# Optimization experiments

Measured on AMD Instinct MI355X. Metric: run time of the kernel, lower is better.

Reference implementation:

```python
import jax, jax.numpy as jnp
import numpy as np

N = 50000      # nodes
E = 800000     # directed edges
GNN_DIM = 128  # node feature dim
HID = 64       # per-head hidden dim of conv1
HEADS = 2
OUT = 16       # output_dim (classes)
TEXT = 500     # tf-idf text dim
M = 10000      # masked / labeled nodes


def setup_inputs() -> dict:
    key = jax.random.key(0)
    ks = jax.random.split(key, 32)
    w = lambda k, s: jax.random.normal(k, s, jnp.float32) * 0.05
    inp = {
        'text_features': jax.random.normal(ks[0], (M, TEXT), jnp.float32),
        'x': jax.random.normal(ks[1], (N, GNN_DIM), jnp.float32),
        'edge_index': jax.random.randint(ks[2], (2, E), 0, N),
        'mask': jax.random.randint(ks[3], (M,), 0, N),
        # text MLP (Linear stored as [in, out])
        'fc1_w': w(ks[4], (TEXT, 128)), 'fc1_b': w(ks[5], (128,)),
        'fc2_w': w(ks[6], (128, 64)),  'fc2_b': w(ks[7], (64,)),
        'fc3_w': w(ks[8], (64, 16)),   'fc3_b': w(ks[9], (16,)),
        'fc4_w': w(ks[10], (16, OUT)), 'fc4_b': w(ks[11], (OUT,)),
        'sc_w': w(ks[12], (TEXT, OUT)), 'sc_b': w(ks[13], (OUT,)),
        # GATConv1: in=GNN_DIM, heads=2, out=HID, concat=True
        'W1': w(ks[14], (GNN_DIM, HEADS * HID)),
        'att_src1': w(ks[15], (HEADS, HID)), 'att_dst1': w(ks[16], (HEADS, HID)),
        'b1': w(ks[17], (HEADS * HID,)),
        # GATConv2: in=2*HID, heads=1, out=OUT, concat=False
        'W2': w(ks[18], (HEADS * HID, OUT)),
        'att_src2': w(ks[19], (1, OUT)), 'att_dst2': w(ks[20], (1, OUT)),
        'b2': w(ks[21], (OUT,)),
        # fc_final: [2*OUT, OUT]
        'fcf_w': w(ks[22], (2 * OUT, OUT)), 'fcf_b': w(ks[23], (OUT,)),
    }
    return inp


def _gat_layer(h_in, src, dst, W, a_src, a_dst, b, heads, dim, concat):
    # PyG GATConv (default negative_slope=0.2, self-loops already appended)
    n = h_in.shape[0]
    h = (h_in @ W).reshape(n, heads, dim)                      # [N,H,D]
    a_s = jnp.einsum('nhd,hd->nh', h, a_src)                   # [N,H]
    a_d = jnp.einsum('nhd,hd->nh', h, a_dst)
    e = jax.nn.leaky_relu(a_s[src] + a_d[dst], 0.2)            # [E,H]
    emax = jax.ops.segment_max(e, dst, num_segments=n)
    ex = jnp.exp(e - emax[dst])
    den = jax.ops.segment_sum(ex, dst, num_segments=n)
    alpha = ex / (den[dst] + 1e-16)                            # [E,H]
    msg = h[src] * alpha[:, :, None]                           # [E,H,D]
    out = jax.ops.segment_sum(msg, dst, num_segments=n)        # [N,H,D]
    out = out.reshape(n, heads * dim) if concat else out.mean(axis=1)
    return out + b


def reference(text_features, x, edge_index, mask,
              fc1_w, fc1_b, fc2_w, fc2_b, fc3_w, fc3_b, fc4_w, fc4_b,
              sc_w, sc_b, W1, att_src1, att_dst1, b1,
              W2, att_src2, att_dst2, b2, fcf_w, fcf_b):
    n = x.shape[0]
    loop = jnp.arange(n, dtype=edge_index.dtype)
    src = jnp.concatenate([edge_index[0], loop])
    dst = jnp.concatenate([edge_index[1], loop])

    # GNN branch
    g = jax.nn.relu(_gat_layer(x, src, dst, W1, att_src1, att_dst1, b1,
                               HEADS, HID, True))
    g = _gat_layer(g, src, dst, W2, att_src2, att_dst2, b2, 1, OUT, False)
    gnn_out = g[mask]                                          # [M,OUT]

    # text MLP branch with shortcut
    t = jax.nn.relu(text_features @ fc1_w + fc1_b)
    t = jax.nn.relu(t @ fc2_w + fc2_b)
    t = jax.nn.relu(t @ fc3_w + fc3_b)
    text_out = (t @ fc4_w + fc4_b) + (text_features @ sc_w + sc_b)  # [M,OUT]

    combined = jnp.concatenate([text_out, gnn_out], axis=1)    # [M,2*OUT]
    return jax.nn.log_softmax(combined @ fcf_w + fcf_b, axis=1)
```

## Files before the change

kernel.cpp:

```cpp
#include <hip/hip_runtime.h>
#include <hip/hip_bf16.h>
#include <cmath>

#define TEXTD 500
#define GNN_DIM 128
#define DEGP(v) ((v) << 5)

typedef __attribute__((ext_vector_type(8))) short bf16x8;
typedef __attribute__((ext_vector_type(4))) float f32x4;

__device__ __forceinline__ float bf2f(unsigned short u) {
    union { unsigned int i; float f; } cv;
    cv.i = ((unsigned int)u) << 16;
    return cv.f;
}
__device__ __forceinline__ unsigned short f2b(float x) {
    __hip_bfloat16 b = __float2bfloat16(x);
    return *reinterpret_cast<unsigned short*>(&b);
}
__device__ __forceinline__ float u2f(unsigned int u) {
    union { unsigned int i; float f; } cv; cv.i = u; return cv.f;
}
__device__ __forceinline__ bf16x8 cvt8(const float* p) {
    float4 u = *(const float4*)p;
    float4 v = *(const float4*)(p + 4);
    bf16x8 f;
    f[0] = (short)f2b(u.x); f[1] = (short)f2b(u.y);
    f[2] = (short)f2b(u.z); f[3] = (short)f2b(u.w);
    f[4] = (short)f2b(v.x); f[5] = (short)f2b(v.y);
    f[6] = (short)f2b(v.z); f[7] = (short)f2b(v.w);
    return f;
}

__global__ __launch_bounds__(256) void setup_kernel(
    int* __restrict__ deg, int N, int NB,
    const float* __restrict__ fc1_w, const float* __restrict__ sc_w,
    const float* __restrict__ W1, const float* __restrict__ W2,
    unsigned short* __restrict__ w1cat, unsigned short* __restrict__ w1g,
    unsigned short* __restrict__ w2t)
{
    if ((int)blockIdx.x < NB) {
        int v = blockIdx.x * 256 + threadIdx.x;
        if (v < N) deg[DEGP(v)] = 0;
        return;
    }
    int idx = (blockIdx.x - NB) * 256 + threadIdx.x;
    if (idx < 144 * 512) {
        int n = idx >> 9, k = idx & 511;
        float v = 0.f;
        if (k < TEXTD) v = (n < 128) ? fc1_w[k * 128 + n] : sc_w[k * 16 + (n - 128)];
        w1cat[idx] = f2b(v);
    } else if (idx < 144 * 512 + 128 * 128) {
        int j = idx - 144 * 512;
        int n = j >> 7, k = j & 127;
        w1g[j] = f2b(W1[k * 128 + n]);
    } else if (idx < 144 * 512 + 128 * 128 + 16 * 128) {
        int j = idx - (144 * 512 + 128 * 128);
        int n = j >> 7, k = j & 127;
        w2t[j] = f2b(W2[k * 16 + n]);
    }
}

__global__ __launch_bounds__(256) void text_fused_kernel(
    const float* __restrict__ text, const short* __restrict__ B,
    const float* __restrict__ fc1_b, const float* __restrict__ sc_b,
    const float* __restrict__ fc2_w, const float* __restrict__ fc2_b,
    const float* __restrict__ fc3_w, const float* __restrict__ fc3_b,
    const float* __restrict__ fc4_w, const float* __restrict__ fc4_b,
    float* __restrict__ text_out, int M)
{
    __shared__ float t1s[64][128];
    __shared__ float tscs[64][16];
    __shared__ float t2s[64][64];
    __shared__ float t3s[64][16];

    const int tid = threadIdx.x;
    const int wave = tid >> 6, lane = tid & 63;
    const int q = lane >> 4, col = lane & 15;
    const int mb = blockIdx.x * 64;
    const int rbase = wave * 16;
    const int arow = min(mb + rbase + col, M - 1);
    const float* ap = text + (size_t)arow * TEXTD + q * 8;

    bf16x8 afrag[16];
    #pragma unroll
    for (int ks = 0; ks < 15; ks++) afrag[ks] = cvt8(ap + ks * 32);
    {
        bf16x8 f;
        int k0 = 480 + q * 8;
        #pragma unroll
        for (int e = 0; e < 8; e++) {
            int k = k0 + e;
            f[e] = (short)((k < TEXTD) ? f2b(text[(size_t)arow * TEXTD + k]) : 0);
        }
        afrag[15] = f;
    }

    for (int nb = 0; nb < 9; nb++) {
        const short* bp = B + (size_t)(nb * 16 + col) * 512 + q * 8;
        f32x4 acc = {0.f, 0.f, 0.f, 0.f};
        #pragma unroll
        for (int ks = 0; ks < 16; ks++)
            acc = __builtin_amdgcn_mfma_f32_16x16x32_bf16(afrag[ks], *(const bf16x8*)(bp + ks * 32), acc, 0, 0, 0);
        #pragma unroll
        for (int i = 0; i < 4; i++) {
            int rl = rbase + q * 4 + i;
            if (nb < 8) t1s[rl][nb * 16 + col] = fmaxf(acc[i] + fc1_b[nb * 16 + col], 0.f);
            else        tscs[rl][col] = acc[i] + sc_b[col];
        }
    }
    __syncthreads();

    const int c2 = tid & 63, rg2 = tid >> 6;
    for (int rb = 0; rb < 16; rb++) {
        int row = rb * 4 + rg2;
        float a2 = fc2_b[c2];
        for (int k = 0; k < 128; k++) a2 = fmaf(t1s[row][k], fc2_w[k * 64 + c2], a2);
        t2s[row][c2] = fmaxf(a2, 0.f);
    }
    __syncthreads();

    const int cs = tid & 15, rg3 = tid >> 4;
    for (int rb = 0; rb < 4; rb++) {
        int row = rb * 16 + rg3;
        float a3 = fc3_b[cs];
        for (int k = 0; k < 64; k++) a3 = fmaf(t2s[row][k], fc3_w[k * 16 + cs], a3);
        t3s[row][cs] = fmaxf(a3, 0.f);
    }
    __syncthreads();

    for (int rb = 0; rb < 4; rb++) {
        int row = rb * 16 + rg3;
        float a4 = fc4_b[cs];
        #pragma unroll
        for (int k = 0; k < 16; k++) a4 = fmaf(t3s[row][k], fc4_w[k * 16 + cs], a4);
        int rg = mb + row;
        if (rg < M) text_out[(size_t)rg * 16 + cs] = a4 + tscs[row][cs];
    }
}

__global__ __launch_bounds__(256) void gemm_h1_kernel(
    const float* __restrict__ x, const short* __restrict__ B,
    const float* __restrict__ as1w, const float* __restrict__ ad1w,
    unsigned short* __restrict__ h1, float* __restrict__ a_s, float* __restrict__ a_d, int N)
{
    const int tid = threadIdx.x;
    const int wave = tid >> 6, lane = tid & 63;
    const int q = lane >> 4, col = lane & 15;
    const int mb = blockIdx.x * 64 + wave * 16;
    const int arow = min(mb + col, N - 1);
    const float* ap = x + (size_t)arow * 128 + q * 8;

    bf16x8 afrag[4];
    #pragma unroll
    for (int ks = 0; ks < 4; ks++) afrag[ks] = cvt8(ap + ks * 32);

    float ps0[4] = {0,0,0,0}, ps1[4] = {0,0,0,0};
    float pd0[4] = {0,0,0,0}, pd1[4] = {0,0,0,0};

    #pragma unroll
    for (int nb = 0; nb < 8; nb++) {
        const short* bp = B + (size_t)(nb * 16 + col) * 128 + q * 8;
        f32x4 acc = {0.f, 0.f, 0.f, 0.f};
        #pragma unroll
        for (int ks = 0; ks < 4; ks++)
            acc = __builtin_amdgcn_mfma_f32_16x16x32_bf16(afrag[ks], *(const bf16x8*)(bp + ks * 32), acc, 0, 0, 0);
        const int j = nb * 16 + col;
        const float asj = as1w[j], adj = ad1w[j];
        #pragma unroll
        for (int i = 0; i < 4; i++) {
            int row = mb + q * 4 + i;
            if (row < N) h1[(size_t)row * 128 + j] = f2b(acc[i]);
            if (nb < 4) { ps0[i] = fmaf(acc[i], asj, ps0[i]); pd0[i] = fmaf(acc[i], adj, pd0[i]); }
            else        { ps1[i] = fmaf(acc[i], asj, ps1[i]); pd1[i] = fmaf(acc[i], adj, pd1[i]); }
        }
    }
    #pragma unroll
    for (int i = 0; i < 4; i++) {
        float v0 = ps0[i], v1 = ps1[i], w0 = pd0[i], w1 = pd1[i];
        #pragma unroll
        for (int off = 1; off < 16; off <<= 1) {
            v0 += __shfl_xor(v0, off, 16);
            v1 += __shfl_xor(v1, off, 16);
            w0 += __shfl_xor(w0, off, 16);
            w1 += __shfl_xor(w1, off, 16);
        }
        int row = mb + q * 4 + i;
        if (col == 0 && row < N) {
            a_s[2 * row] = v0; a_s[2 * row + 1] = v1;
            a_d[2 * row] = w0; a_d[2 * row + 1] = w1;
        }
    }
}

__global__ __launch_bounds__(256) void deg_hist_kernel(
    const int* __restrict__ edst, int* __restrict__ deg, int* __restrict__ rank, int E)
{
    const int base = blockIdx.x * 1024 + threadIdx.x;
    int e0 = base;
    int e1 = base + 256;
    int e2 = base + 512;
    int e3 = base + 768;
    int d0 = (e0 < E) ? edst[e0] : -1;
    int d1 = (e1 < E) ? edst[e1] : -1;
    int d2 = (e2 < E) ? edst[e2] : -1;
    int d3 = (e3 < E) ? edst[e3] : -1;
    int r0 = (d0 >= 0) ? atomicAdd(&deg[DEGP(d0)], 1) : 0;
    int r1 = (d1 >= 0) ? atomicAdd(&deg[DEGP(d1)], 1) : 0;
    int r2 = (d2 >= 0) ? atomicAdd(&deg[DEGP(d2)], 1) : 0;
    int r3 = (d3 >= 0) ? atomicAdd(&deg[DEGP(d3)], 1) : 0;
    if (d0 >= 0) rank[e0] = r0;
    if (d1 >= 0) rank[e1] = r1;
    if (d2 >= 0) rank[e2] = r2;
    if (d3 >= 0) rank[e3] = r3;
}

__global__ __launch_bounds__(256) void part_kernel(
    const int* __restrict__ deg, int* __restrict__ bsum, int N)
{
    const int tid = threadIdx.x;
    int i = blockIdx.x * 256 + tid;
    int d = (i < N) ? deg[DEGP(i)] + 1 : 0;
    #pragma unroll
    for (int off = 32; off > 0; off >>= 1) d += __shfl_down(d, off, 64);
    __shared__ int wsum[4];
    if ((tid & 63) == 0) wsum[tid >> 6] = d;
    __syncthreads();
    if (tid == 0) bsum[blockIdx.x] = wsum[0] + wsum[1] + wsum[2] + wsum[3];
}

__global__ __launch_bounds__(256) void rowptr_kernel(
    const int* __restrict__ deg, const int* __restrict__ bsum,
    int* __restrict__ rowptr, int N, int NB)
{
    __shared__ int bsc[256];
    __shared__ int sc[256];
    const int tid = threadIdx.x;

    int bv = (tid < NB) ? bsum[tid] : 0;
    bsc[tid] = bv;
    for (int off = 1; off < 256; off <<= 1) {
        __syncthreads();
        int t = (tid >= off) ? bsc[tid - off] : 0;
        __syncthreads();
        bsc[tid] += t;
    }
    __syncthreads();
    const int base = (blockIdx.x == 0) ? 0 : bsc[blockIdx.x - 1];

    const int i = blockIdx.x * 256 + tid;
    int d = (i < N) ? deg[DEGP(i)] + 1 : 0;
    sc[tid] = d;
    for (int off = 1; off < 256; off <<= 1) {
        __syncthreads();
        int t = (tid >= off) ? sc[tid - off] : 0;
        __syncthreads();
        sc[tid] += t;
    }
    __syncthreads();
    int incl = sc[tid];
    if (i < N) rowptr[i] = base + incl - d;
    if (i == N - 1) rowptr[N] = base + incl;
}

__device__ __forceinline__ float edge_w(float e) {
    return __expf(e > 0.f ? e : 0.2f * e);
}

__global__ __launch_bounds__(256) void fillw_kernel(
    const int* __restrict__ esrc, const int* __restrict__ edst,
    const int* __restrict__ rank, const int* __restrict__ rowptr,
    uint2* __restrict__ eslot,
    const float* __restrict__ a_s, const float* __restrict__ a_d, int E, int N)
{
    int e = blockIdx.x * 256 + threadIdx.x;
    if (e < E) {
        int src = esrc[e], dst = edst[e];
        int pos = rowptr[dst] + 1 + rank[e];
        float2 as = *(const float2*)(a_s + 2 * src);
        float2 ad = *(const float2*)(a_d + 2 * dst);
        unsigned int w0 = f2b(edge_w(as.x + ad.x));
        unsigned int w1 = f2b(edge_w(as.y + ad.y));
        uint2 o; o.x = (unsigned int)src; o.y = (w1 << 16) | w0;
        eslot[pos] = o;
    } else if (e < E + N) {
        int v = e - E;
        float2 as = *(const float2*)(a_s + 2 * v);
        float2 ad = *(const float2*)(a_d + 2 * v);
        unsigned int w0 = f2b(edge_w(as.x + ad.x));
        unsigned int w1 = f2b(edge_w(as.y + ad.y));
        uint2 o; o.x = (unsigned int)v; o.y = (w1 << 16) | w0;
        eslot[rowptr[v]] = o;
    }
}

template<int B>
__device__ __forceinline__ void gat1_batch(
    int i0, int end, int endm1, int wsh,
    const uint2* __restrict__ eslot, const uint2* __restrict__ h1u, unsigned int dp,
    float& a0, float& a1, float& a2, float& a3, float& den)
{
    int ics[B];
    uint2 sl[B];
    float wv[B];
    uint2 hv[B];
    #pragma unroll
    for (int k = 0; k < B; k++) ics[k] = min(i0 + 2 * k, endm1);
    #pragma unroll
    for (int k = 0; k < B; k++) sl[k] = eslot[ics[k]];
    #pragma unroll
    for (int k = 0; k < B; k++) {
        float w = u2f((sl[k].y << wsh) & 0xffff0000u);
        wv[k] = (i0 + 2 * k < end) ? w : 0.f;
    }
    #pragma unroll
    for (int k = 0; k < B; k++) hv[k] = h1u[(sl[k].x << 5) | dp];
    #pragma unroll
    for (int k = 0; k < B; k++) {
        float w = wv[k];
        den += w;
        a0 = fmaf(w, u2f(hv[k].x << 16),          a0);
        a1 = fmaf(w, u2f(hv[k].x & 0xffff0000u),  a1);
        a2 = fmaf(w, u2f(hv[k].y << 16),          a2);
        a3 = fmaf(w, u2f(hv[k].y & 0xffff0000u),  a3);
    }
}

__global__ __launch_bounds__(256) void gat1_gather_kernel(
    const int* __restrict__ rowptr, const uint2* __restrict__ eslot,
    const uint2* __restrict__ h1u,
    const float* __restrict__ b1, uint2* __restrict__ g1b, int N)
{
    const int v = blockIdx.x * 4 + (threadIdx.x >> 6);
    if (v >= N) return;
    const int lane = threadIdx.x & 63;
    const int slot = lane >> 5;
    const unsigned int dp = lane & 31;
    const int head = dp >> 4;
    const int wsh = head ? 0 : 16;
    const int beg = rowptr[v], end = rowptr[v + 1];
    const int deg = end - beg;
    const int endm1 = end - 1;
    const int i0 = beg + slot;

    float a0 = 0.f, a1 = 0.f, a2 = 0.f, a3 = 0.f, den = 0.f;

    if (deg <= 8) {
        gat1_batch<4>(i0, end, endm1, wsh, eslot, h1u, dp, a0, a1, a2, a3, den);
    } else {
        gat1_batch<8>(i0, end, endm1, wsh, eslot, h1u, dp, a0, a1, a2, a3, den);
        for (int base = i0 + 16; base < end; base += 8)
            gat1_batch<4>(base, end, endm1, wsh, eslot, h1u, dp, a0, a1, a2, a3, den);
    }

    a0 += __shfl_xor(a0, 32, 64);
    a1 += __shfl_xor(a1, 32, 64);
    a2 += __shfl_xor(a2, 32, 64);
    a3 += __shfl_xor(a3, 32, 64);
    den += __shfl_xor(den, 32, 64);

    if (lane < 32) {
        float inv = 1.f / (den + 1e-16f);
        float4 bv = *(const float4*)(b1 + 4 * dp);
        float o0 = fmaxf(fmaf(a0, inv, bv.x), 0.f);
        float o1 = fmaxf(fmaf(a1, inv, bv.y), 0.f);
        float o2 = fmaxf(fmaf(a2, inv, bv.z), 0.f);
        float o3 = fmaxf(fmaf(a3, inv, bv.w), 0.f);
        uint2 o;
        o.x = ((unsigned int)f2b(o1) << 16) | f2b(o0);
        o.y = ((unsigned int)f2b(o3) << 16) | f2b(o2);
        g1b[((unsigned int)v << 5) | dp] = o;
    }
}

__global__ __launch_bounds__(256) void gat2_proj_kernel(
    const unsigned short* __restrict__ g1b, const short* __restrict__ w2t,
    const float* __restrict__ as2w, const float* __restrict__ ad2w,
    float* __restrict__ h2, float* __restrict__ a_s2, float* __restrict__ a_d2, int N)
{
    const int tid = threadIdx.x;
    const int wave = tid >> 6, lane = tid & 63;
    const int q = lane >> 4, col = lane & 15;
    const int mb = blockIdx.x * 64 + wave * 16;
    const int arow = min(mb + col, N - 1);
    const short* ap = (const short*)g1b + (size_t)arow * 128 + q * 8;
    const short* bp = w2t + (size_t)col * 128 + q * 8;

    f32x4 acc = {0.f, 0.f, 0.f, 0.f};
    #pragma unroll
    for (int ks = 0; ks < 4; ks++)
        acc = __builtin_amdgcn_mfma_f32_16x16x32_bf16(
            *(const bf16x8*)(ap + ks * 32), *(const bf16x8*)(bp + ks * 32), acc, 0, 0, 0);

    const float asj = as2w[col], adj = ad2w[col];
    #pragma unroll
    for (int i = 0; i < 4; i++) {
        int row = mb + q * 4 + i;
        float ps = acc[i] * asj, pd = acc[i] * adj;
        #pragma unroll
        for (int off = 1; off < 16; off <<= 1) {
            ps += __shfl_xor(ps, off, 16);
            pd += __shfl_xor(pd, off, 16);
        }
        if (row < N) {
            h2[(size_t)row * 16 + col] = acc[i];
            if (col == 0) { a_s2[row] = ps; a_d2[row] = pd; }
        }
    }
}

__global__ __launch_bounds__(256) void gat2_final_kernel(
    const int* __restrict__ rowptr, const uint2* __restrict__ eslot,
    const float* __restrict__ h2,
    const float* __restrict__ a_s2, const float* __restrict__ a_d2,
    const float* __restrict__ b2, const int* __restrict__ mask,
    const float* __restrict__ text_out,
    const float* __restrict__ fcf_w, const float* __restrict__ fcf_b,
    float* __restrict__ out, int M)
{
    const int tid = threadIdx.x;
    const int m = blockIdx.x * 4 + (tid >> 6);
    if (m >= M) return;
    const int lane = tid & 63, slot = lane >> 4, c = lane & 15;
    const int v = mask[m];
    const float adv = a_d2[v];
    const int beg = rowptr[v], end = rowptr[v + 1];
    const int i0 = beg + slot;

    float acc = 0.f, den = 0.f;
    unsigned int idxs[8];
    float msk[8], as_[8], hval[8];
    #pragma unroll
    for (int k = 0; k < 8; k++) {
        int i = i0 + 4 * k;
        int ic = min(i, end - 1);
        idxs[k] = eslot[ic].x;
        msk[k] = (i < end) ? 1.f : 0.f;
    }
    #pragma unroll
    for (int k = 0; k < 8; k++) as_[k] = a_s2[idxs[k]];
    #pragma unroll
    for (int k = 0; k < 8; k++) hval[k] = h2[(idxs[k] << 4) | (unsigned)c];
    #pragma unroll
    for (int k = 0; k < 8; k++) {
        float e = as_[k] + adv;
        float w = msk[k] * __expf(e > 0.f ? e : 0.2f * e);
        den += w;
        acc = fmaf(w, hval[k], acc);
    }
    for (int i = i0 + 32; i < end; i += 4) {
        unsigned int src = eslot[i].x;
        float e = a_s2[src] + adv;
        float w = __expf(e > 0.f ? e : 0.2f * e);
        den += w;
        acc = fmaf(w, h2[(src << 4) | (unsigned)c], acc);
    }

    acc += __shfl_xor(acc, 16, 64);
    acc += __shfl_xor(acc, 32, 64);
    den += __shfl_xor(den, 16, 64);
    den += __shfl_xor(den, 32, 64);

    if (slot == 0) {
        float gval = acc / (den + 1e-16f) + b2[c];
        float tval = text_out[(size_t)m * 16 + c];

        float logit = fcf_b[c];
        #pragma unroll
        for (int k = 0; k < 16; k++) {
            logit = fmaf(__shfl(tval, k, 16), fcf_w[k * 16 + c], logit);
            logit = fmaf(__shfl(gval, k, 16), fcf_w[(16 + k) * 16 + c], logit);
        }
        float mx = logit;
        #pragma unroll
        for (int off = 8; off > 0; off >>= 1) mx = fmaxf(mx, __shfl_xor(mx, off, 16));
        float se = expf(logit - mx);
        #pragma unroll
        for (int off = 8; off > 0; off >>= 1) se += __shfl_xor(se, off, 16);
        out[(size_t)m * 16 + c] = logit - mx - logf(se);
    }
}

extern "C" void kernel_launch(void* const* d_in, const int* in_sizes, int n_in,
                              void* d_out, int out_size, void* d_ws, size_t ws_size,
                              hipStream_t stream)
{
    const float* text  = (const float*)d_in[0];
    const float* x     = (const float*)d_in[1];
    const int*   ei    = (const int*)  d_in[2];
    const int*   mask  = (const int*)  d_in[3];
    const float* fc1_w = (const float*)d_in[4];  const float* fc1_b = (const float*)d_in[5];
    const float* fc2_w = (const float*)d_in[6];  const float* fc2_b = (const float*)d_in[7];
    const float* fc3_w = (const float*)d_in[8];  const float* fc3_b = (const float*)d_in[9];
    const float* fc4_w = (const float*)d_in[10]; const float* fc4_b = (const float*)d_in[11];
    const float* sc_w  = (const float*)d_in[12]; const float* sc_b  = (const float*)d_in[13];
    const float* W1    = (const float*)d_in[14];
    const float* as1w  = (const float*)d_in[15]; const float* ad1w  = (const float*)d_in[16];
    const float* b1    = (const float*)d_in[17];
    const float* W2    = (const float*)d_in[18];
    const float* as2w  = (const float*)d_in[19]; const float* ad2w  = (const float*)d_in[20];
    const float* b2    = (const float*)d_in[21];
    const float* fcf_w = (const float*)d_in[22]; const float* fcf_b = (const float*)d_in[23];

    const int M  = in_sizes[3];
    const int N  = in_sizes[1] / GNN_DIM;
    const int E  = in_sizes[2] / 2;
    const int EP = E + N;
    const int* esrc = ei;
    const int* edst = ei + E;

    const int Mp = ((M + 63) / 64) * 64;
    const int Np = ((N + 63) / 64) * 64;
    const int NB = (N + 255) / 256;

    float* ws = (float*)d_ws;
    size_t off = 0;
    auto alloc = [&](size_t n) { float* p = ws + off; off += (n + 63) & ~size_t(63); return p; };

    unsigned short* h1    = (unsigned short*)alloc((size_t)Np * 64);
    unsigned int*   g1b   = (unsigned int*)  alloc((size_t)N * 64);
    unsigned short* w1cat = (unsigned short*)alloc(144 * 256);
    unsigned short* w1g   = (unsigned short*)alloc(128 * 64);
    unsigned short* w2t   = (unsigned short*)alloc(16 * 64);
    float* a_s1     = alloc((size_t)2 * N);
    float* a_d1     = alloc((size_t)2 * N);
    float* h2       = alloc((size_t)N * 16);
    float* a_s2     = alloc(N);
    float* a_d2     = alloc(N);
    float* text_out = alloc((size_t)M * 16);
    uint2* eslot    = (uint2*)alloc((size_t)2 * EP);
    int* deg        = (int*)alloc((size_t)N * 32);
    int* rank       = (int*)alloc(E);
    int* rowptr     = (int*)alloc(N + 1);
    int* bsum       = (int*)alloc(256);

    const int convBlocks = (144 * 512 + 128 * 128 + 16 * 128 + 255) / 256;

    setup_kernel<<<NB + convBlocks, 256, 0, stream>>>(
        deg, N, NB, fc1_w, sc_w, W1, W2, w1cat, w1g, w2t);

    deg_hist_kernel<<<(E + 1023) / 1024, 256, 0, stream>>>(edst, deg, rank, E);
    part_kernel<<<NB, 256, 0, stream>>>(deg, bsum, N);
    rowptr_kernel<<<NB, 256, 0, stream>>>(deg, bsum, rowptr, N, NB);

    gemm_h1_kernel<<<Np / 64, 256, 0, stream>>>(
        x, (const short*)w1g, as1w, ad1w, h1, a_s1, a_d1, N);

    fillw_kernel<<<(E + N + 255) / 256, 256, 0, stream>>>(
        esrc, edst, rank, rowptr, eslot, a_s1, a_d1, E, N);

    text_fused_kernel<<<Mp / 64, 256, 0, stream>>>(
        text, (const short*)w1cat, fc1_b, sc_b,
        fc2_w, fc2_b, fc3_w, fc3_b, fc4_w, fc4_b, text_out, M);

    gat1_gather_kernel<<<(N + 3) / 4, 256, 0, stream>>>(
        rowptr, eslot, (const uint2*)h1, b1, (uint2*)g1b, N);

    gat2_proj_kernel<<<Np / 64, 256, 0, stream>>>(
        (const unsigned short*)g1b, (const short*)w2t, as2w, ad2w, h2, a_s2, a_d2, N);

    gat2_final_kernel<<<(M + 3) / 4, 256, 0, stream>>>(
        rowptr, eslot, h2, a_s2, a_d2, b2, mask, text_out, fcf_w, fcf_b,
        (float*)d_out, M);
}
```

Measured before the change: 189.3 us.

## Run text MLP layers fc2-fc4 on MFMA with one-wave blocks

Replaces the scalar FMA loops for fc2, fc3 and fc4 in the text branch with bf16 MFMA tiles. The transposed bf16 weights for these layers are prepared in the setup kernel. The text kernel is reshaped to one 64-thread wave per 16 rows, with bf16 intermediates held in small padded LDS buffers. This is meant to cut the scalar-ALU-bound tail of the text MLP and raise block count. In exchange it adds bf16 rounding to the intermediate activations and runs 625 blocks of a single wave each.

```diff
diff --git a/kernel.cpp b/kernel.cpp
--- a/kernel.cpp
+++ b/kernel.cpp
@@ -36,8 +36,11 @@
     int* __restrict__ deg, int N, int NB,
     const float* __restrict__ fc1_w, const float* __restrict__ sc_w,
     const float* __restrict__ W1, const float* __restrict__ W2,
+    const float* __restrict__ fc2_w, const float* __restrict__ fc3_w,
+    const float* __restrict__ fc4_w,
     unsigned short* __restrict__ w1cat, unsigned short* __restrict__ w1g,
-    unsigned short* __restrict__ w2t)
+    unsigned short* __restrict__ w2t, unsigned short* __restrict__ fc2t,
+    unsigned short* __restrict__ fc3t, unsigned short* __restrict__ fc4t)
 {
     if ((int)blockIdx.x < NB) {
         int v = blockIdx.x * 256 + threadIdx.x;
@@ -45,41 +48,51 @@
         return;
     }
     int idx = (blockIdx.x - NB) * 256 + threadIdx.x;
-    if (idx < 144 * 512) {
+    if (idx < 73728) {
         int n = idx >> 9, k = idx & 511;
         float v = 0.f;
         if (k < TEXTD) v = (n < 128) ? fc1_w[k * 128 + n] : sc_w[k * 16 + (n - 128)];
         w1cat[idx] = f2b(v);
-    } else if (idx < 144 * 512 + 128 * 128) {
-        int j = idx - 144 * 512;
+    } else if (idx < 90112) {
+        int j = idx - 73728;
         int n = j >> 7, k = j & 127;
         w1g[j] = f2b(W1[k * 128 + n]);
-    } else if (idx < 144 * 512 + 128 * 128 + 16 * 128) {
-        int j = idx - (144 * 512 + 128 * 128);
+    } else if (idx < 92160) {
+        int j = idx - 90112;
         int n = j >> 7, k = j & 127;
         w2t[j] = f2b(W2[k * 16 + n]);
-    }
-}
-
-__global__ __launch_bounds__(256) void text_fused_kernel(
-    const float* __restrict__ text, const short* __restrict__ B,
+    } else if (idx < 100352) {
+        int j = idx - 92160;
+        int n = j >> 7, k = j & 127;
+        fc2t[j] = f2b(fc2_w[k * 64 + n]);
+    } else if (idx < 101376) {
+        int j = idx - 100352;
+        int n = j >> 6, k = j & 63;
+        fc3t[j] = f2b(fc3_w[k * 16 + n]);
+    } else if (idx < 101888) {
+        int j = idx - 101376;
+        int n = j >> 5, k = j & 31;
+        fc4t[j] = f2b((k < 16) ? fc4_w[k * 16 + n] : 0.f);
+    }
+}
+
+__global__ __launch_bounds__(64) void text_mfma_kernel(
+    const float* __restrict__ text, const short* __restrict__ w1cat,
     const float* __restrict__ fc1_b, const float* __restrict__ sc_b,
-    const float* __restrict__ fc2_w, const float* __restrict__ fc2_b,
-    const float* __restrict__ fc3_w, const float* __restrict__ fc3_b,
-    const float* __restrict__ fc4_w, const float* __restrict__ fc4_b,
+    const short* __restrict__ fc2t, const float* __restrict__ fc2_b,
+    const short* __restrict__ fc3t, const float* __restrict__ fc3_b,
+    const short* __restrict__ fc4t, const float* __restrict__ fc4_b,
     float* __restrict__ text_out, int M)
 {
-    __shared__ float t1s[64][128];
-    __shared__ float tscs[64][16];
-    __shared__ float t2s[64][64];
-    __shared__ float t3s[64][16];
-
-    const int tid = threadIdx.x;
-    const int wave = tid >> 6, lane = tid & 63;
+    __shared__ unsigned short t1b[16 * 136];
+    __shared__ unsigned short t2b[16 * 72];
+    __shared__ unsigned short t3b[16 * 40];
+    __shared__ float tscs[16 * 16];
+
+    const int lane = threadIdx.x;
     const int q = lane >> 4, col = lane & 15;
-    const int mb = blockIdx.x * 64;
-    const int rbase = wave * 16;
-    const int arow = min(mb + rbase + col, M - 1);
+    const int mb = blockIdx.x * 16;
+    const int arow = min(mb + col, M - 1);
     const float* ap = text + (size_t)arow * TEXTD + q * 8;
 
     bf16x8 afrag[16];
@@ -97,45 +110,66 @@
     }
 
     for (int nb = 0; nb < 9; nb++) {
-        const short* bp = B + (size_t)(nb * 16 + col) * 512 + q * 8;
+        const short* bp = w1cat + (size_t)(nb * 16 + col) * 512 + q * 8;
         f32x4 acc = {0.f, 0.f, 0.f, 0.f};
         #pragma unroll
         for (int ks = 0; ks < 16; ks++)
             acc = __builtin_amdgcn_mfma_f32_16x16x32_bf16(afrag[ks], *(const bf16x8*)(bp + ks * 32), acc, 0, 0, 0);
         #pragma unroll
         for (int i = 0; i < 4; i++) {
-            int rl = rbase + q * 4 + i;
-            if (nb < 8) t1s[rl][nb * 16 + col] = fmaxf(acc[i] + fc1_b[nb * 16 + col], 0.f);
-            else        tscs[rl][col] = acc[i] + sc_b[col];
+            int row = q * 4 + i;
+            if (nb < 8) t1b[row * 136 + nb * 16 + col] = f2b(fmaxf(acc[i] + fc1_b[nb * 16 + col], 0.f));
+            else        tscs[row * 16 + col] = acc[i] + sc_b[col];
         }
     }
     __syncthreads();
 
-    const int c2 = tid & 63, rg2 = tid >> 6;
-    for (int rb = 0; rb < 16; rb++) {
-        int row = rb * 4 + rg2;
-        float a2 = fc2_b[c2];
-        for (int k = 0; k < 128; k++) a2 = fmaf(t1s[row][k], fc2_w[k * 64 + c2], a2);
-        t2s[row][c2] = fmaxf(a2, 0.f);
+    const unsigned short* a2p = t1b + col * 136 + q * 8;
+    #pragma unroll
+    for (int nt = 0; nt < 4; nt++) {
+        const short* bp = fc2t + (nt * 16 + col) * 128 + q * 8;
+        f32x4 acc = {0.f, 0.f, 0.f, 0.f};
+        #pragma unroll
+        for (int ks = 0; ks < 4; ks++)
+            acc = __builtin_amdgcn_mfma_f32_16x16x32_bf16(
+                *(const bf16x8*)(a2p + ks * 32), *(const bf16x8*)(bp + ks * 32), acc, 0, 0, 0);
+        #pragma unroll
+        for (int i = 0; i < 4; i++) {
+            int row = q * 4 + i;
+            t2b[row * 72 + nt * 16 + col] = f2b(fmaxf(acc[i] + fc2_b[nt * 16 + col], 0.f));
+        }
     }
     __syncthreads();
 
-    const int cs = tid & 15, rg3 = tid >> 4;
-    for (int rb = 0; rb < 4; rb++) {
-        int row = rb * 16 + rg3;
-        float a3 = fc3_b[cs];
-        for (int k = 0; k < 64; k++) a3 = fmaf(t2s[row][k], fc3_w[k * 16 + cs], a3);
-        t3s[row][cs] = fmaxf(a3, 0.f);
+    {
+        const unsigned short* a3p = t2b + col * 72 + q * 8;
+        const short* bp = fc3t + col * 64 + q * 8;
+        f32x4 acc = {0.f, 0.f, 0.f, 0.f};
+        #pragma unroll
+        for (int ks = 0; ks < 2; ks++)
+            acc = __builtin_amdgcn_mfma_f32_16x16x32_bf16(
+                *(const bf16x8*)(a3p + ks * 32), *(const bf16x8*)(bp + ks * 32), acc, 0, 0, 0);
+        #pragma unroll
+        for (int i = 0; i < 4; i++) {
+            int row = q * 4 + i;
+            t3b[row * 40 + col] = f2b(fmaxf(acc[i] + fc3_b[col], 0.f));
+            t3b[row * 40 + 16 + col] = 0;
+        }
     }
     __syncthreads();
 
-    for (int rb = 0; rb < 4; rb++) {
-        int row = rb * 16 + rg3;
-        float a4 = fc4_b[cs];
-        #pragma unroll
-        for (int k = 0; k < 16; k++) a4 = fmaf(t3s[row][k], fc4_w[k * 16 + cs], a4);
-        int rg = mb + row;
-        if (rg < M) text_out[(size_t)rg * 16 + cs] = a4 + tscs[row][cs];
+    {
+        const unsigned short* a4p = t3b + col * 40 + q * 8;
+        const short* bp = fc4t + col * 32 + q * 8;
+        f32x4 acc = {0.f, 0.f, 0.f, 0.f};
+        acc = __builtin_amdgcn_mfma_f32_16x16x32_bf16(
+            *(const bf16x8*)a4p, *(const bf16x8*)bp, acc, 0, 0, 0);
+        #pragma unroll
+        for (int i = 0; i < 4; i++) {
+            int row = q * 4 + i;
+            int rg = mb + row;
+            if (rg < M) text_out[(size_t)rg * 16 + col] = acc[i] + fc4_b[col] + tscs[row * 16 + col];
+        }
     }
 }
 
@@ -509,7 +543,6 @@
     const int* esrc = ei;
     const int* edst = ei + E;
 
-    const int Mp = ((M + 63) / 64) * 64;
     const int Np = ((N + 63) / 64) * 64;
     const int NB = (N + 255) / 256;
 
@@ -522,6 +555,9 @@
     unsigned short* w1cat = (unsigned short*)alloc(144 * 256);
     unsigned short* w1g   = (unsigned short*)alloc(128 * 64);
     unsigned short* w2t   = (unsigned short*)alloc(16 * 64);
+    unsigned short* fc2t  = (unsigned short*)alloc(64 * 64);
+    unsigned short* fc3t  = (unsigned short*)alloc(16 * 32);
+    unsigned short* fc4t  = (unsigned short*)alloc(16 * 16);
     float* a_s1     = alloc((size_t)2 * N);
     float* a_d1     = alloc((size_t)2 * N);
     float* h2       = alloc((size_t)N * 16);
@@ -534,10 +570,11 @@
     int* rowptr     = (int*)alloc(N + 1);
     int* bsum       = (int*)alloc(256);
 
-    const int convBlocks = (144 * 512 + 128 * 128 + 16 * 128 + 255) / 256;
+    const int convBlocks = (101888 + 255) / 256;
 
     setup_kernel<<<NB + convBlocks, 256, 0, stream>>>(
-        deg, N, NB, fc1_w, sc_w, W1, W2, w1cat, w1g, w2t);
+        deg, N, NB, fc1_w, sc_w, W1, W2, fc2_w, fc3_w, fc4_w,
+        w1cat, w1g, w2t, fc2t, fc3t, fc4t);
 
     deg_hist_kernel<<<(E + 1023) / 1024, 256, 0, stream>>>(edst, deg, rank, E);
     part_kernel<<<NB, 256, 0, stream>>>(deg, bsum, N);
@@ -549,9 +586,10 @@
     fillw_kernel<<<(E + N + 255) / 256, 256, 0, stream>>>(
         esrc, edst, rank, rowptr, eslot, a_s1, a_d1, E, N);
 
-    text_fused_kernel<<<Mp / 64, 256, 0, stream>>>(
+    text_mfma_kernel<<<(M + 15) / 16, 64, 0, stream>>>(
         text, (const short*)w1cat, fc1_b, sc_b,
-        fc2_w, fc2_b, fc3_w, fc3_b, fc4_w, fc4_b, text_out, M);
+        (const short*)fc2t, fc2_b, (const short*)fc3t, fc3_b,
+        (const short*)fc4t, fc4_b, text_out, M);
 
     gat1_gather_kernel<<<(N + 3) / 4, 256, 0, stream>>>(
         rowptr, eslot, (const uint2*)h1, b1, (uint2*)g1b, N);
```

After: 182.0 us. 3.9% less time.
